# Kernel tuning notes

Measured on AMD Instinct MI355X. Metric: run time of the kernel, lower is better.

The kernel has to match this reference:

```python
import jax, jax.numpy as jnp
import numpy as np

HIDDEN = 1024
NUM_HEADS = 16
DK = 64  # key_and_query_dim
DV = 64  # value_dim
NEG_INF = -1.0e9


def setup_inputs() -> dict:
    key = jax.random.key(0)
    ks = jax.random.split(key, 12)
    B, S = 4, 2048
    scale = 0.02
    return {
        "q_hidden_inputs": jax.random.normal(ks[0], (B, S, HIDDEN), dtype=jnp.float32),
        "k_hidden_inputs": jax.random.normal(ks[1], (B, S, HIDDEN), dtype=jnp.float32),
        "v_hidden_inputs": jax.random.normal(ks[2], (B, S, HIDDEN), dtype=jnp.float32),
        "mask": jax.random.randint(ks[3], (B, S, S), 0, 2) > 0,
        # per-head projection weights, stacked over heads: [H, hidden, dk/dv]
        "wq": jax.random.normal(ks[4], (NUM_HEADS, HIDDEN, DK), dtype=jnp.float32) * scale,
        "bq": jax.random.normal(ks[5], (NUM_HEADS, DK), dtype=jnp.float32) * scale,
        "wk": jax.random.normal(ks[6], (NUM_HEADS, HIDDEN, DK), dtype=jnp.float32) * scale,
        "bk": jax.random.normal(ks[7], (NUM_HEADS, DK), dtype=jnp.float32) * scale,
        "wv": jax.random.normal(ks[8], (NUM_HEADS, HIDDEN, DV), dtype=jnp.float32) * scale,
        "bv": jax.random.normal(ks[9], (NUM_HEADS, DV), dtype=jnp.float32) * scale,
        # output projection: [H*dv, hidden]
        "wo": jax.random.normal(ks[10], (NUM_HEADS * DV, HIDDEN), dtype=jnp.float32) * scale,
        "bo": jax.random.normal(ks[11], (HIDDEN,), dtype=jnp.float32) * scale,
    }


def reference(q_hidden_inputs, k_hidden_inputs, v_hidden_inputs, mask,
              wq, bq, wk, bk, wv, bv, wo, bo):
    # Per-head linear projections, vectorized over heads: [B, H, S, dk]
    q = jnp.einsum('bsd,hdk->bhsk', q_hidden_inputs, wq) + bq[None, :, None, :]
    k = jnp.einsum('bsd,hdk->bhsk', k_hidden_inputs, wk) + bk[None, :, None, :]
    v = jnp.einsum('bsd,hdv->bhsv', v_hidden_inputs, wv) + bv[None, :, None, :]
    # scores: [B, H, Sq, Sk]
    scores = jnp.einsum('bhsk,bhtk->bhst', q, k) / jnp.sqrt(jnp.float32(DK))
    scores = jnp.where(mask[:, None, :, :], scores, NEG_INF)
    attn = jax.nn.softmax(scores, axis=-1)
    out = jnp.einsum('bhst,bhtv->bhsv', attn, v)  # [B, H, Sq, dv]
    B, H, Sq, Dv = out.shape
    # heads concatenated along last dim in head order (same as torch.cat)
    out = jnp.transpose(out, (0, 2, 1, 3)).reshape(B, Sq, H * Dv)
    return out @ wo + bo
```

## Files before the change

### kernel.cpp

```cpp
#include <hip/hip_runtime.h>
#include <stdint.h>


typedef __bf16 bf16x8_t __attribute__((ext_vector_type(8)));
typedef float f32x4_t __attribute__((ext_vector_type(4)));

#define HID   1024
#define SLEN  2048
#define BATCH 4
#define NH    16
#define MROWS 8192
#define L2E   1.44269504f

__device__ __forceinline__ unsigned short bfbits(float f) {
  union { __bf16 h; unsigned short u; } v; v.h = (__bf16)f; return v.u;
}
__device__ __forceinline__ unsigned int packbf(float a, float b) {
  return (unsigned int)bfbits(a) | ((unsigned int)bfbits(b) << 16);
}
__device__ __forceinline__ float fast_exp2(float x) {
#if __has_builtin(__builtin_amdgcn_exp2f)
  return __builtin_amdgcn_exp2f(x);
#else
  return __exp2f(x);
#endif
}

__device__ __forceinline__ void gload_lds16(const void* g, void* l) {
  __builtin_amdgcn_global_load_lds((const __attribute__((address_space(1))) void*)g,
                                   (__attribute__((address_space(3))) void*)l,
                                   16, 0, 0);
}

__device__ __forceinline__ bf16x8_t frag_ld(const unsigned short* lds, int row, int sblk) {
  int sp = sblk ^ (row & 7);
  return *(const bf16x8_t*)(lds + (row << 6) + (sp << 3));
}

__global__ void detect_mask_kernel(const unsigned int* __restrict__ m,
                                   unsigned int* __restrict__ flag) {
  unsigned int v = m[threadIdx.x];
  unsigned long long b = __ballot(v > 1u);
  if (threadIdx.x == 0) flag[0] = 0u;
  __syncthreads();
  if ((threadIdx.x & 63) == 0 && b) atomicOr(flag, 1u);
}

__global__ __launch_bounds__(256) void mask_bits_kernel(const void* __restrict__ maskp,
    const unsigned int* __restrict__ flag, unsigned long long* __restrict__ bits) {
  int lane = threadIdx.x & 63, wv = threadIdx.x >> 6;
  bool bytemask = flag[0] != 0u;
  size_t w0 = (size_t)blockIdx.x * 64 + (size_t)wv * 16;
  for (int it = 0; it < 16; ++it) {
    size_t word = w0 + it;
    unsigned int v;
    if (bytemask) v = ((const unsigned char*)maskp)[word * 64 + lane];
    else          v = ((const unsigned int*)maskp)[word * 64 + lane];
    unsigned long long bm = __ballot(v != 0u);
    if (lane == 0) bits[word] = bm;
  }
}

__global__ __launch_bounds__(256) void cvt_x_kernel(const float* __restrict__ src,
                                                    unsigned short* __restrict__ xb) {
  size_t base = (size_t)blockIdx.x * 1024 + (size_t)threadIdx.x * 4;
  float4 v = *(const float4*)(src + base);
  ushort4 o;
  o.x = bfbits(v.x); o.y = bfbits(v.y); o.z = bfbits(v.z); o.w = bfbits(v.w);
  *(ushort4*)(xb + base) = o;
}

__global__ __launch_bounds__(256) void pack_w_kernel(const float* __restrict__ wq,
    const float* __restrict__ wk, const float* __restrict__ wv,
    const float* __restrict__ wo, unsigned short* __restrict__ wt) {
  int z = blockIdx.y;
  int id = blockIdx.x * 256 + threadIdx.x;
  int n = id >> 8;
  int d0 = (id & 255) << 2;
  ushort4 o;
  if (z < 3) {
    const float* w = z == 0 ? wq : (z == 1 ? wk : wv);
    const float* base = w + (size_t)(n >> 6) * (HID * 64) + (n & 63);
    o.x = bfbits(base[(size_t)(d0 + 0) * 64]);
    o.y = bfbits(base[(size_t)(d0 + 1) * 64]);
    o.z = bfbits(base[(size_t)(d0 + 2) * 64]);
    o.w = bfbits(base[(size_t)(d0 + 3) * 64]);
  } else {
    o.x = bfbits(wo[(size_t)(d0 + 0) * HID + n]);
    o.y = bfbits(wo[(size_t)(d0 + 1) * HID + n]);
    o.z = bfbits(wo[(size_t)(d0 + 2) * HID + n]);
    o.w = bfbits(wo[(size_t)(d0 + 3) * HID + n]);
  }
  *(ushort4*)(wt + (size_t)z * (HID * HID) + (size_t)n * HID + d0) = o;
}

__device__ __forceinline__ void gemm_tile_mainloop(const unsigned short* __restrict__ A,
    const unsigned short* __restrict__ B, unsigned short* lA, unsigned short* lB,
    int tid, f32x4_t (&acc)[4][4]) {
  int lane = tid & 63, w = tid >> 6;
  int wr = (w >> 1) << 6, wc = (w & 1) << 6;
  for (int kt = 0; kt < HID; kt += 64) {
    __syncthreads();
#pragma unroll
    for (int i = 0; i < 4; ++i) {
      int flat = i * 256 + tid;
      int row = flat >> 3;
      int sl = (flat & 7) ^ (row & 7);
      unsigned short* la = lA + ((i * 256 + w * 64) << 3);
      unsigned short* lb = lB + ((i * 256 + w * 64) << 3);
      gload_lds16(A + (size_t)row * HID + kt + sl * 8, la);
      gload_lds16(B + (size_t)row * HID + kt + sl * 8, lb);
    }
    __syncthreads();
#pragma unroll
    for (int kk = 0; kk < 2; ++kk) {
      bf16x8_t af[4], bfr[4];
#pragma unroll
      for (int mi = 0; mi < 4; ++mi)
        af[mi] = frag_ld(lA, wr + mi * 16 + (lane & 15), kk * 4 + (lane >> 4));
#pragma unroll
      for (int ni = 0; ni < 4; ++ni)
        bfr[ni] = frag_ld(lB, wc + ni * 16 + (lane & 15), kk * 4 + (lane >> 4));
#pragma unroll
      for (int mi = 0; mi < 4; ++mi)
#pragma unroll
        for (int ni = 0; ni < 4; ++ni)
          acc[mi][ni] = __builtin_amdgcn_mfma_f32_16x16x32_bf16(af[mi], bfr[ni],
                                                                acc[mi][ni], 0, 0, 0);
    }
  }
}

__global__ __launch_bounds__(256) void gemm_qkv_kernel(
    const unsigned short* __restrict__ Ain, const unsigned short* __restrict__ Bin,
    const float* __restrict__ bias, unsigned short* __restrict__ Out, float scale) {
  __shared__ __align__(16) unsigned short lA[128 * 64];
  __shared__ __align__(16) unsigned short lB[128 * 64];
  int m0 = blockIdx.x * 128, n0 = blockIdx.y * 128;
  const unsigned short* A = Ain + (size_t)m0 * HID;
  const unsigned short* B = Bin + (size_t)n0 * HID;
  f32x4_t acc[4][4] = {};
  int tid = threadIdx.x;
  gemm_tile_mainloop(A, B, lA, lB, tid, acc);
  int lane = tid & 63, w = tid >> 6;
  int wr = (w >> 1) << 6, wc = (w & 1) << 6;
#pragma unroll
  for (int mi = 0; mi < 4; ++mi)
#pragma unroll
    for (int ni = 0; ni < 4; ++ni) {
      int col = n0 + wc + ni * 16 + (lane & 15);
      float bb = bias[col];
      int h = col >> 6, d = col & 63;
#pragma unroll
      for (int r = 0; r < 4; ++r) {
        int row = m0 + wr + mi * 16 + ((lane >> 4) << 2) + r;
        int b = row >> 11, s = row & 2047;
        Out[((((size_t)b * NH + h) * SLEN + s) << 6) + d] = bfbits((acc[mi][ni][r] + bb) * scale);
      }
    }
}

__global__ __launch_bounds__(256) void gemm_out_kernel(
    const unsigned short* __restrict__ Ob, const unsigned short* __restrict__ WoT,
    const float* __restrict__ bo, float* __restrict__ out) {
  __shared__ __align__(16) unsigned short lA[128 * 64];
  __shared__ __align__(16) unsigned short lB[128 * 64];
  int m0 = blockIdx.x * 128, n0 = blockIdx.y * 128;
  const unsigned short* A = Ob + (size_t)m0 * HID;
  const unsigned short* B = WoT + (size_t)n0 * HID;
  f32x4_t acc[4][4] = {};
  int tid = threadIdx.x;
  gemm_tile_mainloop(A, B, lA, lB, tid, acc);
  int lane = tid & 63, w = tid >> 6;
  int wr = (w >> 1) << 6, wc = (w & 1) << 6;
#pragma unroll
  for (int mi = 0; mi < 4; ++mi)
#pragma unroll
    for (int ni = 0; ni < 4; ++ni) {
      int col = n0 + wc + ni * 16 + (lane & 15);
      float bb = bo[col];
#pragma unroll
      for (int r = 0; r < 4; ++r) {
        int row = m0 + wr + mi * 16 + ((lane >> 4) << 2) + r;
        out[(size_t)row * HID + col] = acc[mi][ni][r] + bb;
      }
    }
}

__global__ __launch_bounds__(256) void attn_kernel(
    const unsigned short* __restrict__ Q, const unsigned short* __restrict__ K,
    const unsigned short* __restrict__ V, const unsigned long long* __restrict__ mbits,
    unsigned short* __restrict__ O) {
  __shared__ __align__(16) unsigned short lK[64 * 64];
  __shared__ __align__(16) unsigned short lV[64 * 64];
  __shared__ __align__(16) unsigned short lP[128 * 64];
  int tid = threadIdx.x, lane = tid & 63, w = tid >> 6;
  int g = lane >> 4, ql = lane & 15;
  int bid = blockIdx.x;
  int bh = (bid & 7) * 8 + ((bid >> 3) >> 4);
  int qt = (bid >> 3) & 15;
  int b = bh >> 4, h = bh & 15;
  int q0 = qt * 128;
  const unsigned short* Qb = Q + (size_t)bh * (SLEN * 64);
  const unsigned short* Kb = K + (size_t)bh * (SLEN * 64);
  const unsigned short* Vb = V + (size_t)bh * (SLEN * 64);
  const unsigned long long* Mrow = mbits + (size_t)b * SLEN * 32;

  bf16x8_t qf[2][2];
#pragma unroll
  for (int mi = 0; mi < 2; ++mi)
#pragma unroll
    for (int kk = 0; kk < 2; ++kk) {
      int row = q0 + w * 32 + mi * 16 + ql;
      qf[mi][kk] = *(const bf16x8_t*)(Qb + (size_t)row * 64 + kk * 32 + g * 8);
    }

  bf16x8_t onesf;
#pragma unroll
  for (int e = 0; e < 8; ++e) onesf[e] = (__bf16)1.0f;

  f32x4_t aco[2][4] = {};
  f32x4_t slacc[2] = {};

  for (int kt = 0; kt < SLEN / 64; ++kt) {
    __syncthreads();
#pragma unroll
    for (int i = 0; i < 2; ++i) {
      int flat = i * 256 + tid;
      int row = flat >> 3;
      int sl = (flat & 7) ^ (row & 7);
      gload_lds16(Kb + (size_t)(kt * 64 + row) * 64 + sl * 8, lK + ((i * 256 + w * 64) << 3));
    }
    {
      int kvp = tid >> 3;
      int dv0 = (tid & 7) << 3;
      const unsigned short* vs = Vb + (size_t)(kt * 64 + kvp * 2) * 64 + dv0;
      bf16x8_t v0 = *(const bf16x8_t*)(vs);
      bf16x8_t v1 = *(const bf16x8_t*)(vs + 64);
      union { __bf16 b[8]; unsigned short u[8]; } a0, a1;
      *(bf16x8_t*)a0.b = v0; *(bf16x8_t*)a1.b = v1;
#pragma unroll
      for (int e = 0; e < 8; ++e) {
        int dv = dv0 + e;
        unsigned int val = (unsigned int)a0.u[e] | ((unsigned int)a1.u[e] << 16);
        int sp2 = (kvp >> 2) ^ (dv & 7);
        *(unsigned int*)((char*)lV + dv * 128 + sp2 * 16 + (kvp & 3) * 4) = val;
      }
    }
    __syncthreads();

    f32x4_t st[2][4];
#pragma unroll
    for (int mi = 0; mi < 2; ++mi)
#pragma unroll
      for (int ni = 0; ni < 4; ++ni) st[mi][ni] = (f32x4_t){0.f, 0.f, 0.f, 0.f};
#pragma unroll
    for (int kk = 0; kk < 2; ++kk) {
      bf16x8_t kf[4];
#pragma unroll
      for (int ni = 0; ni < 4; ++ni)
        kf[ni] = frag_ld(lK, ni * 16 + ql, kk * 4 + g);
#pragma unroll
      for (int mi = 0; mi < 2; ++mi)
#pragma unroll
        for (int ni = 0; ni < 4; ++ni)
          st[mi][ni] = __builtin_amdgcn_mfma_f32_16x16x32_bf16(kf[ni], qf[mi][kk],
                                                               st[mi][ni], 0, 0, 0);
    }

#pragma unroll
    for (int mi = 0; mi < 2; ++mi) {
      int qrow = q0 + w * 32 + mi * 16 + ql;
      unsigned long long bg = Mrow[(size_t)qrow * 32 + kt] >> (4 * g);
      int prow = w * 32 + mi * 16 + ql;
#pragma unroll
      for (int ni = 0; ni < 4; ++ni) {
        float p[4];
#pragma unroll
        for (int r = 0; r < 4; ++r) {
          float e = fast_exp2(st[mi][ni][r]);
          p[r] = ((unsigned int)(bg >> (16 * ni + r)) & 1u) ? e : 0.f;
        }
        unsigned int lo = packbf(p[0], p[1]);
        unsigned int hi = packbf(p[2], p[3]);
        int sl = (2 * ni + (g >> 1)) ^ (prow & 7);
        *(uint2*)((char*)lP + prow * 128 + sl * 16 + (g & 1) * 8) = make_uint2(lo, hi);
      }
    }

#pragma unroll
    for (int kk2 = 0; kk2 < 2; ++kk2) {
      bf16x8_t vf[4];
#pragma unroll
      for (int dvf = 0; dvf < 4; ++dvf)
        vf[dvf] = frag_ld(lV, dvf * 16 + ql, kk2 * 4 + g);
#pragma unroll
      for (int mi = 0; mi < 2; ++mi) {
        bf16x8_t pf = frag_ld(lP, w * 32 + mi * 16 + ql, kk2 * 4 + g);
        slacc[mi] = __builtin_amdgcn_mfma_f32_16x16x32_bf16(onesf, pf, slacc[mi], 0, 0, 0);
#pragma unroll
        for (int dvf = 0; dvf < 4; ++dvf)
          aco[mi][dvf] = __builtin_amdgcn_mfma_f32_16x16x32_bf16(vf[dvf], pf,
                                                                 aco[mi][dvf], 0, 0, 0);
      }
    }
  }

#pragma unroll
  for (int mi = 0; mi < 2; ++mi) {
    float inv = 1.0f / slacc[mi][0];
    int prow = w * 32 + mi * 16 + ql;
#pragma unroll
    for (int dvf = 0; dvf < 4; ++dvf) {
      unsigned int lo = packbf(aco[mi][dvf][0] * inv, aco[mi][dvf][1] * inv);
      unsigned int hi = packbf(aco[mi][dvf][2] * inv, aco[mi][dvf][3] * inv);
      int sl = (2 * dvf + (g >> 1)) ^ (prow & 7);
      *(uint2*)((char*)lP + prow * 128 + sl * 16 + (g & 1) * 8) = make_uint2(lo, hi);
    }
  }
#pragma unroll
  for (int it = 0; it < 8; ++it) {
    int rloc = g + 4 * it;
    int row = w * 32 + rloc;
    int sl = (ql >> 1) ^ (row & 7);
    uint2 v = *(const uint2*)((const char*)lP + row * 128 + sl * 16 + (ql & 1) * 8);
    int qrow = q0 + row;
    *(uint2*)(O + (((size_t)b * SLEN + qrow) << 10) + h * 64 + ql * 4) = v;
  }
}

extern "C" void kernel_launch(void* const* d_in, const int* in_sizes, int n_in,
                              void* d_out, int out_size, void* d_ws, size_t ws_size,
                              hipStream_t stream) {
  (void)in_sizes; (void)n_in; (void)out_size; (void)ws_size;
  const float* xq = (const float*)d_in[0];
  const float* xk = (const float*)d_in[1];
  const float* xv = (const float*)d_in[2];
  const void*  mask = d_in[3];
  const float* wq = (const float*)d_in[4];
  const float* bq = (const float*)d_in[5];
  const float* wk = (const float*)d_in[6];
  const float* bk = (const float*)d_in[7];
  const float* wv = (const float*)d_in[8];
  const float* bv = (const float*)d_in[9];
  const float* wo = (const float*)d_in[10];
  const float* bo = (const float*)d_in[11];
  float* out = (float*)d_out;

  char* ws = (char*)d_ws;
  unsigned short* XbZ  = (unsigned short*)(ws);
  unsigned short* Ob   = (unsigned short*)(ws);
  unsigned short* Wt   = (unsigned short*)(ws + 16777216ull);
  unsigned short* QKV  = (unsigned short*)(ws + 25165824ull);
  unsigned int*   flag = (unsigned int*)(ws + 75497472ull);
  unsigned long long* mbits = (unsigned long long*)d_out;

  const float* xs[3]   = {xq, xk, xv};
  const float* bias[3] = {bq, bk, bv};

  detect_mask_kernel<<<1, 256, 0, stream>>>((const unsigned int*)mask, flag);
  mask_bits_kernel<<<4096, 256, 0, stream>>>(mask, flag, mbits);
  pack_w_kernel<<<dim3(1024, 4), 256, 0, stream>>>(wq, wk, wv, wo, Wt);
  for (int z = 0; z < 3; ++z) {
    cvt_x_kernel<<<8192, 256, 0, stream>>>(xs[z], XbZ);
    gemm_qkv_kernel<<<dim3(64, 8), 256, 0, stream>>>(
        XbZ, Wt + (size_t)z * (HID * HID), bias[z],
        QKV + (size_t)z * ((size_t)MROWS * 1024), z == 0 ? 0.125f * L2E : 1.0f);
  }
  attn_kernel<<<1024, 256, 0, stream>>>(QKV, QKV + 8388608ull,
                                        QKV + 16777216ull, mbits, Ob);
  gemm_out_kernel<<<dim3(64, 8), 256, 0, stream>>>(Ob, Wt + 3ull * (HID * HID), bo, out);
}
```

Before: 332.7 us.

## Double-buffer LDS tiles in GEMM and attention loops to overlap loads

Splits the LDS tiles in the GEMM mainloop and the attention K/V loop into two buffers. The next tile is prefetched into the alternate buffer while MFMAs run on the current one, which leaves one barrier per iteration instead of two. In attention, the next V tile is held in registers and written transposed into LDS after the PV product. This costs twice the LDS and more registers, which may lower occupancy, and the lP buffer is still shared by all waves across iterations.

```diff
diff --git a/kernel.cpp b/kernel.cpp
--- a/kernel.cpp
+++ b/kernel.cpp
@@ -94,33 +94,41 @@
   *(ushort4*)(wt + (size_t)z * (HID * HID) + (size_t)n * HID + d0) = o;
 }
 
+__device__ __forceinline__ void gemm_stage(const unsigned short* __restrict__ A,
+    const unsigned short* __restrict__ B, unsigned short* la, unsigned short* lb,
+    int tid, int w, int kt) {
+#pragma unroll
+  for (int i = 0; i < 4; ++i) {
+    int flat = i * 256 + tid;
+    int row = flat >> 3;
+    int sl = (flat & 7) ^ (row & 7);
+    gload_lds16(A + (size_t)row * HID + kt + sl * 8, la + ((i * 256 + w * 64) << 3));
+    gload_lds16(B + (size_t)row * HID + kt + sl * 8, lb + ((i * 256 + w * 64) << 3));
+  }
+}
+
 __device__ __forceinline__ void gemm_tile_mainloop(const unsigned short* __restrict__ A,
-    const unsigned short* __restrict__ B, unsigned short* lA, unsigned short* lB,
-    int tid, f32x4_t (&acc)[4][4]) {
+    const unsigned short* __restrict__ B, unsigned short (*lA)[128 * 64],
+    unsigned short (*lB)[128 * 64], int tid, f32x4_t (&acc)[4][4]) {
   int lane = tid & 63, w = tid >> 6;
   int wr = (w >> 1) << 6, wc = (w & 1) << 6;
+  gemm_stage(A, B, lA[0], lB[0], tid, w, 0);
+  __syncthreads();
+  int cur = 0;
   for (int kt = 0; kt < HID; kt += 64) {
-    __syncthreads();
-#pragma unroll
-    for (int i = 0; i < 4; ++i) {
-      int flat = i * 256 + tid;
-      int row = flat >> 3;
-      int sl = (flat & 7) ^ (row & 7);
-      unsigned short* la = lA + ((i * 256 + w * 64) << 3);
-      unsigned short* lb = lB + ((i * 256 + w * 64) << 3);
-      gload_lds16(A + (size_t)row * HID + kt + sl * 8, la);
-      gload_lds16(B + (size_t)row * HID + kt + sl * 8, lb);
-    }
-    __syncthreads();
+    if (kt + 64 < HID)
+      gemm_stage(A, B, lA[cur ^ 1], lB[cur ^ 1], tid, w, kt + 64);
+    const unsigned short* la = lA[cur];
+    const unsigned short* lb = lB[cur];
 #pragma unroll
     for (int kk = 0; kk < 2; ++kk) {
       bf16x8_t af[4], bfr[4];
 #pragma unroll
       for (int mi = 0; mi < 4; ++mi)
-        af[mi] = frag_ld(lA, wr + mi * 16 + (lane & 15), kk * 4 + (lane >> 4));
+        af[mi] = frag_ld(la, wr + mi * 16 + (lane & 15), kk * 4 + (lane >> 4));
 #pragma unroll
       for (int ni = 0; ni < 4; ++ni)
-        bfr[ni] = frag_ld(lB, wc + ni * 16 + (lane & 15), kk * 4 + (lane >> 4));
+        bfr[ni] = frag_ld(lb, wc + ni * 16 + (lane & 15), kk * 4 + (lane >> 4));
 #pragma unroll
       for (int mi = 0; mi < 4; ++mi)
 #pragma unroll
@@ -128,14 +136,16 @@
           acc[mi][ni] = __builtin_amdgcn_mfma_f32_16x16x32_bf16(af[mi], bfr[ni],
                                                                 acc[mi][ni], 0, 0, 0);
     }
+    __syncthreads();
+    cur ^= 1;
   }
 }
 
 __global__ __launch_bounds__(256) void gemm_qkv_kernel(
     const unsigned short* __restrict__ Ain, const unsigned short* __restrict__ Bin,
     const float* __restrict__ bias, unsigned short* __restrict__ Out, float scale) {
-  __shared__ __align__(16) unsigned short lA[128 * 64];
-  __shared__ __align__(16) unsigned short lB[128 * 64];
+  __shared__ __align__(16) unsigned short lA[2][128 * 64];
+  __shared__ __align__(16) unsigned short lB[2][128 * 64];
   int m0 = blockIdx.x * 128, n0 = blockIdx.y * 128;
   const unsigned short* A = Ain + (size_t)m0 * HID;
   const unsigned short* B = Bin + (size_t)n0 * HID;
@@ -163,8 +173,8 @@
 __global__ __launch_bounds__(256) void gemm_out_kernel(
     const unsigned short* __restrict__ Ob, const unsigned short* __restrict__ WoT,
     const float* __restrict__ bo, float* __restrict__ out) {
-  __shared__ __align__(16) unsigned short lA[128 * 64];
-  __shared__ __align__(16) unsigned short lB[128 * 64];
+  __shared__ __align__(16) unsigned short lA[2][128 * 64];
+  __shared__ __align__(16) unsigned short lB[2][128 * 64];
   int m0 = blockIdx.x * 128, n0 = blockIdx.y * 128;
   const unsigned short* A = Ob + (size_t)m0 * HID;
   const unsigned short* B = WoT + (size_t)n0 * HID;
@@ -191,8 +201,8 @@
     const unsigned short* __restrict__ Q, const unsigned short* __restrict__ K,
     const unsigned short* __restrict__ V, const unsigned long long* __restrict__ mbits,
     unsigned short* __restrict__ O) {
-  __shared__ __align__(16) unsigned short lK[64 * 64];
-  __shared__ __align__(16) unsigned short lV[64 * 64];
+  __shared__ __align__(16) unsigned short lK[2][64 * 64];
+  __shared__ __align__(16) unsigned short lV[2][64 * 64];
   __shared__ __align__(16) unsigned short lP[128 * 64];
   int tid = threadIdx.x, lane = tid & 63, w = tid >> 6;
   int g = lane >> 4, ql = lane & 15;
@@ -206,6 +216,9 @@
   const unsigned short* Vb = V + (size_t)bh * (SLEN * 64);
   const unsigned long long* Mrow = mbits + (size_t)b * SLEN * 32;
 
+  int kvp = tid >> 3;
+  int dv0 = (tid & 7) << 3;
+
   bf16x8_t qf[2][2];
 #pragma unroll
   for (int mi = 0; mi < 2; ++mi)
@@ -222,33 +235,49 @@
   f32x4_t aco[2][4] = {};
   f32x4_t slacc[2] = {};
 
+#pragma unroll
+  for (int i = 0; i < 2; ++i) {
+    int flat = i * 256 + tid;
+    int row = flat >> 3;
+    int sl = (flat & 7) ^ (row & 7);
+    gload_lds16(Kb + (size_t)row * 64 + sl * 8, lK[0] + ((i * 256 + w * 64) << 3));
+  }
+  {
+    const unsigned short* vs = Vb + (size_t)(kvp * 2) * 64 + dv0;
+    bf16x8_t v0 = *(const bf16x8_t*)(vs);
+    bf16x8_t v1 = *(const bf16x8_t*)(vs + 64);
+    union { __bf16 b[8]; unsigned short u[8]; } a0, a1;
+    *(bf16x8_t*)a0.b = v0; *(bf16x8_t*)a1.b = v1;
+#pragma unroll
+    for (int e = 0; e < 8; ++e) {
+      int dv = dv0 + e;
+      unsigned int val = (unsigned int)a0.u[e] | ((unsigned int)a1.u[e] << 16);
+      int sp2 = (kvp >> 2) ^ (dv & 7);
+      *(unsigned int*)((char*)lV[0] + dv * 128 + sp2 * 16 + (kvp & 3) * 4) = val;
+    }
+  }
+  __syncthreads();
+
+  int cur = 0;
   for (int kt = 0; kt < SLEN / 64; ++kt) {
-    __syncthreads();
-#pragma unroll
-    for (int i = 0; i < 2; ++i) {
-      int flat = i * 256 + tid;
-      int row = flat >> 3;
-      int sl = (flat & 7) ^ (row & 7);
-      gload_lds16(Kb + (size_t)(kt * 64 + row) * 64 + sl * 8, lK + ((i * 256 + w * 64) << 3));
-    }
-    {
-      int kvp = tid >> 3;
-      int dv0 = (tid & 7) << 3;
-      const unsigned short* vs = Vb + (size_t)(kt * 64 + kvp * 2) * 64 + dv0;
-      bf16x8_t v0 = *(const bf16x8_t*)(vs);
-      bf16x8_t v1 = *(const bf16x8_t*)(vs + 64);
-      union { __bf16 b[8]; unsigned short u[8]; } a0, a1;
-      *(bf16x8_t*)a0.b = v0; *(bf16x8_t*)a1.b = v1;
-#pragma unroll
-      for (int e = 0; e < 8; ++e) {
-        int dv = dv0 + e;
-        unsigned int val = (unsigned int)a0.u[e] | ((unsigned int)a1.u[e] << 16);
-        int sp2 = (kvp >> 2) ^ (dv & 7);
-        *(unsigned int*)((char*)lV + dv * 128 + sp2 * 16 + (kvp & 3) * 4) = val;
-      }
-    }
-    __syncthreads();
-
+    bf16x8_t vn0, vn1;
+    bool pre = (kt + 1) < SLEN / 64;
+    if (pre) {
+#pragma unroll
+      for (int i = 0; i < 2; ++i) {
+        int flat = i * 256 + tid;
+        int row = flat >> 3;
+        int sl = (flat & 7) ^ (row & 7);
+        gload_lds16(Kb + (size_t)((kt + 1) * 64 + row) * 64 + sl * 8,
+                    lK[cur ^ 1] + ((i * 256 + w * 64) << 3));
+      }
+      const unsigned short* vs = Vb + (size_t)((kt + 1) * 64 + kvp * 2) * 64 + dv0;
+      vn0 = *(const bf16x8_t*)(vs);
+      vn1 = *(const bf16x8_t*)(vs + 64);
+    }
+
+    const unsigned short* kbuf = lK[cur];
+    const unsigned short* vbuf = lV[cur];
     f32x4_t st[2][4];
 #pragma unroll
     for (int mi = 0; mi < 2; ++mi)
@@ -259,7 +288,7 @@
       bf16x8_t kf[4];
 #pragma unroll
       for (int ni = 0; ni < 4; ++ni)
-        kf[ni] = frag_ld(lK, ni * 16 + ql, kk * 4 + g);
+        kf[ni] = frag_ld(kbuf, ni * 16 + ql, kk * 4 + g);
 #pragma unroll
       for (int mi = 0; mi < 2; ++mi)
 #pragma unroll
@@ -293,7 +322,7 @@
       bf16x8_t vf[4];
 #pragma unroll
       for (int dvf = 0; dvf < 4; ++dvf)
-        vf[dvf] = frag_ld(lV, dvf * 16 + ql, kk2 * 4 + g);
+        vf[dvf] = frag_ld(vbuf, dvf * 16 + ql, kk2 * 4 + g);
 #pragma unroll
       for (int mi = 0; mi < 2; ++mi) {
         bf16x8_t pf = frag_ld(lP, w * 32 + mi * 16 + ql, kk2 * 4 + g);
@@ -304,6 +333,20 @@
                                                                  aco[mi][dvf], 0, 0, 0);
       }
     }
+
+    if (pre) {
+      union { __bf16 b[8]; unsigned short u[8]; } a0, a1;
+      *(bf16x8_t*)a0.b = vn0; *(bf16x8_t*)a1.b = vn1;
+#pragma unroll
+      for (int e = 0; e < 8; ++e) {
+        int dv = dv0 + e;
+        unsigned int val = (unsigned int)a0.u[e] | ((unsigned int)a1.u[e] << 16);
+        int sp2 = (kvp >> 2) ^ (dv & 7);
+        *(unsigned int*)((char*)lV[cur ^ 1] + dv * 128 + sp2 * 16 + (kvp & 3) * 4) = val;
+      }
+    }
+    __syncthreads();
+    cur ^= 1;
   }
 
 #pragma unroll
```

Measured after the change: 315.8 us. 1.05x faster.
